# Kernel optimization log

Measured on AMD Instinct MI355X. Metric: run time of the kernel, lower is better.

The kernel has to match this reference:

```python
import jax, jax.numpy as jnp
import numpy as np

D_MODEL = 1024
NUM_HEADS = 16
HEAD_DIM = D_MODEL // NUM_HEADS


def setup_inputs() -> dict:
    key = jax.random.key(0)
    ks = jax.random.split(key, 11)
    B, S = 2, 2048
    s = 1.0 / np.sqrt(D_MODEL)
    return {
        "q": jax.random.normal(ks[0], (B, S, D_MODEL), jnp.float32),
        "k": jax.random.normal(ks[1], (B, S, D_MODEL), jnp.float32),
        "v": jax.random.normal(ks[2], (B, S, D_MODEL), jnp.float32),
        "Wq": jax.random.normal(ks[3], (D_MODEL, D_MODEL), jnp.float32) * s,
        "bq": jnp.zeros((D_MODEL,), jnp.float32),
        "Wk": jax.random.normal(ks[4], (D_MODEL, D_MODEL), jnp.float32) * s,
        "bk": jnp.zeros((D_MODEL,), jnp.float32),
        "Wv": jax.random.normal(ks[5], (D_MODEL, D_MODEL), jnp.float32) * s,
        "bv": jnp.zeros((D_MODEL,), jnp.float32),
        "Wo": jax.random.normal(ks[6], (D_MODEL, D_MODEL), jnp.float32) * s,
        "bo": jnp.zeros((D_MODEL,), jnp.float32),
    }


def _split_heads(x):
    B, S, _ = x.shape
    return x.reshape(B, S, NUM_HEADS, HEAD_DIM).transpose(0, 2, 1, 3)  # [B,H,S,Dh]


def reference(q, k, v, Wq, bq, Wk, bk, Wv, bv, Wo, bo):
    B, S, _ = q.shape
    qh = _split_heads(q @ Wq.T + bq)
    kh = _split_heads(k @ Wk.T + bk)
    vh = _split_heads(v @ Wv.T + bv)
    scale = 1.0 / jnp.sqrt(jnp.asarray(HEAD_DIM, qh.dtype))
    scores = jnp.einsum("bhqd,bhkd->bhqk", qh, kh) * scale  # [B,H,S,S]
    attn = jax.nn.softmax(scores, axis=-1)
    out = jnp.einsum("bhqk,bhkd->bhqd", attn, vh)
    out = out.transpose(0, 2, 1, 3).reshape(B, S, D_MODEL)
    return out @ Wo.T + bo
```

## Files before the change

kernel.cpp:

```cpp
#include <hip/hip_runtime.h>
#include <cstdint>
#include <cstddef>

#define DEVI __device__ __forceinline__

typedef short bf16x8 __attribute__((ext_vector_type(8)));
typedef short bf16x4 __attribute__((ext_vector_type(4)));
typedef float f32x4 __attribute__((ext_vector_type(4)));
typedef float f32x16 __attribute__((ext_vector_type(16)));
typedef unsigned short u16x4 __attribute__((ext_vector_type(4)));

constexpr int D_MODEL = 1024;
constexpr int HEADS = 16;
constexpr int DH = 64;
constexpr int SEQ = 2048;
constexpr int KDIM = 1024;

DEVI unsigned short f2bf(float f) {
  union { float f; unsigned u; } v; v.f = f;
  unsigned r = v.u + 0x7fffu + ((v.u >> 16) & 1u);
  return (unsigned short)(r >> 16);
}

DEVI unsigned pkbf(float a, float b) {
  return __builtin_amdgcn_perm(__float_as_uint(b), __float_as_uint(a), 0x07060302u);
}

DEVI void cp16(const void* g, void* l) {
  __builtin_amdgcn_global_load_lds(
      (const __attribute__((address_space(1))) void*)g,
      (__attribute__((address_space(3))) void*)l, 16, 0, 0);
}

DEVI f32x16 mfma_32x32x8(bf16x4 a, bf16x4 b, f32x16 c) {
#if __has_builtin(__builtin_amdgcn_mfma_f32_32x32x8bf16_1k)
  return __builtin_amdgcn_mfma_f32_32x32x8bf16_1k(a, b, c, 0, 0, 0);
#else
  asm volatile("v_mfma_f32_32x32x8_bf16 %0, %1, %2, %0" : "+v"(c) : "v"(a), "v"(b));
  return c;
#endif
}

__global__ void __launch_bounds__(256) castall(
    const float* __restrict__ q, const float* __restrict__ k, const float* __restrict__ v,
    const float* __restrict__ Wq, const float* __restrict__ Wk,
    const float* __restrict__ Wv, const float* __restrict__ Wo,
    unsigned short* __restrict__ qb, unsigned short* __restrict__ kb, unsigned short* __restrict__ vb,
    unsigned short* __restrict__ Wqb, unsigned short* __restrict__ Wkb,
    unsigned short* __restrict__ Wvb, unsigned short* __restrict__ Wob) {
  int bid = blockIdx.x;
  const float* s; unsigned short* d; int off;
  if (bid < 12288) {
    int w = bid >> 12; off = bid & 4095;
    s = (w == 0) ? q : ((w == 1) ? k : v);
    d = (w == 0) ? qb : ((w == 1) ? kb : vb);
  } else {
    int w = (bid - 12288) >> 10; off = bid & 1023;
    s = (w == 0) ? Wq : ((w == 1) ? Wk : ((w == 2) ? Wv : Wo));
    d = (w == 0) ? Wqb : ((w == 1) ? Wkb : ((w == 2) ? Wvb : Wob));
  }
  int i = (off * 256 + threadIdx.x) * 4;
  float4 x = *(const float4*)(s + i);
  u16x4 o; o[0] = f2bf(x.x); o[1] = f2bf(x.y); o[2] = f2bf(x.z); o[3] = f2bf(x.w);
  *(u16x4*)(d + i) = o;
}

DEVI void gemm_body64(const unsigned short* __restrict__ A, const unsigned short* __restrict__ W,
                      const float* __restrict__ bias, unsigned short* __restrict__ obf,
                      float* __restrict__ of32, float oscale, int mode, int bm, int bn,
                      unsigned short* As, unsigned short* Bs) {
  const int tid = threadIdx.x, lane = tid & 63, wave = tid >> 6;
  const int l16 = lane & 15, quad = lane >> 4;
  const int wn = wave * 32;
  const int sw = (l16 >> 1) & 3;
  f32x4 acc[4][2] = {};

  for (int k0 = 0; k0 < KDIM; k0 += 32) {
    {
      int row = tid >> 2, pblk = tid & 3;
      int col = (pblk ^ ((row >> 1) & 3)) * 8;
      cp16(A + (size_t)(bm * 64 + row) * KDIM + k0 + col, &As[tid * 8]);
    }
#pragma unroll
    for (int c = 0; c < 2; ++c) {
      int slot = c * 256 + tid;
      int row = slot >> 2, pblk = slot & 3;
      int col = (pblk ^ ((row >> 1) & 3)) * 8;
      cp16(W + (size_t)(bn * 128 + row) * KDIM + k0 + col, &Bs[slot * 8]);
    }
    asm volatile("s_waitcnt vmcnt(0)" ::: "memory");
    __syncthreads();
    bf16x8 af[4], bfr[2];
#pragma unroll
    for (int t = 0; t < 4; ++t)
      af[t] = *(const bf16x8*)&As[(t * 16 + l16) * 32 + ((quad ^ sw) * 8)];
#pragma unroll
    for (int u = 0; u < 2; ++u)
      bfr[u] = *(const bf16x8*)&Bs[(wn + u * 16 + l16) * 32 + ((quad ^ sw) * 8)];
#pragma unroll
    for (int i = 0; i < 4; ++i)
#pragma unroll
      for (int j = 0; j < 2; ++j)
        acc[i][j] = __builtin_amdgcn_mfma_f32_16x16x32_bf16(af[i], bfr[j], acc[i][j], 0, 0, 0);
    __syncthreads();
  }

#pragma unroll
  for (int i = 0; i < 4; ++i) {
#pragma unroll
    for (int j = 0; j < 2; ++j) {
      const int col = bn * 128 + wn + j * 16 + l16;
      const float bv = bias[col];
#pragma unroll
      for (int r = 0; r < 4; ++r) {
        const int row = bm * 64 + i * 16 + quad * 4 + r;
        const float val = (acc[i][j][r] + bv) * oscale;
        if (mode == 2) {
          of32[(size_t)row * D_MODEL + col] = val;
        } else {
          const int b = row >> 11, s = row & (SEQ - 1);
          const int h = col >> 6, d = col & (DH - 1);
          size_t idx;
          if (mode == 0) idx = ((size_t)(b * HEADS + h) * SEQ + s) * DH + d;
          else           idx = ((size_t)(b * HEADS + h) * DH + d) * SEQ + s;
          obf[idx] = f2bf(val);
        }
      }
    }
  }
}

__global__ void __launch_bounds__(256) qkv_gemm(
    const unsigned short* __restrict__ qb, const unsigned short* __restrict__ kb,
    const unsigned short* __restrict__ vb,
    const unsigned short* __restrict__ Wqb, const unsigned short* __restrict__ Wkb,
    const unsigned short* __restrict__ Wvb,
    const float* __restrict__ bq, const float* __restrict__ bk, const float* __restrict__ bv,
    unsigned short* __restrict__ Qh, unsigned short* __restrict__ Kh,
    unsigned short* __restrict__ Vt, float qscale) {
  __shared__ unsigned short As[64 * 32], Bs[128 * 32];
  const int bid = blockIdx.x, seg = bid >> 9, inner = bid & 511;
  const int bm = inner >> 3, bn = inner & 7;
  const unsigned short* A = (seg == 0) ? qb : ((seg == 1) ? kb : vb);
  const unsigned short* W = (seg == 0) ? Wqb : ((seg == 1) ? Wkb : Wvb);
  const float* bias = (seg == 0) ? bq : ((seg == 1) ? bk : bv);
  unsigned short* O = (seg == 0) ? Qh : ((seg == 1) ? Kh : Vt);
  gemm_body64(A, W, bias, O, nullptr, (seg == 0) ? qscale : 1.0f, (seg == 2) ? 1 : 0, bm, bn, As, Bs);
}

__global__ void __launch_bounds__(256) out_gemm(const unsigned short* __restrict__ AO,
                                                const unsigned short* __restrict__ Wob,
                                                const float* __restrict__ bo,
                                                float* __restrict__ out) {
  __shared__ unsigned short As[64 * 32], Bs[128 * 32];
  const int bid = blockIdx.x, bm = bid >> 3, bn = bid & 7;
  gemm_body64(AO, Wob, bo, nullptr, out, 1.0f, 2, bm, bn, As, Bs);
}

__global__ void __launch_bounds__(256) attn(const unsigned short* __restrict__ Qh,
                                            const unsigned short* __restrict__ Kh,
                                            const unsigned short* __restrict__ Vt,
                                            unsigned short* __restrict__ AO) {
  __shared__ __align__(16) char smem[32768];
  unsigned short* Ks = (unsigned short*)smem;
  unsigned short* Vs = (unsigned short*)(smem + 16384);

  const int bid = blockIdx.x;
  const int qt = bid >> 5, head = bid & 31, b = head >> 4, h = head & 15;
  const int tid = threadIdx.x;
  const int lane = tid & 63, wave = tid >> 6;
  const int wq = wave >> 1, wk = wave & 1;
  const int l31 = lane & 31, hh = lane >> 5;

  const unsigned short* Qhead = Qh + (size_t)(b * HEADS + h) * SEQ * DH;
  const unsigned short* Khead = Kh + (size_t)(b * HEADS + h) * SEQ * DH;
  const unsigned short* Vhead = Vt + (size_t)(b * HEADS + h) * DH * SEQ;

  const int qrow = qt * 64 + wq * 32 + l31;
  bf16x8 aq[4];
#pragma unroll
  for (int it = 0; it < 4; ++it)
    aq[it] = *(const bf16x8*)&Qhead[(size_t)qrow * DH + it * 16 + hh * 8];

  f32x16 oacc[2] = {};
  float lsum = 0.f;

  for (int kc = 0; kc < SEQ / 128; ++kc) {
#pragma unroll
    for (int c = 0; c < 4; ++c) {
      int s = c * 256 + tid;
      int row = s >> 3, pblk = s & 7;
      int jb = pblk ^ (row & 7);
      cp16(Khead + (size_t)(kc * 128 + row) * DH + jb * 8, &Ks[s * 8]);
    }
#pragma unroll
    for (int c = 0; c < 4; ++c) {
      int s = c * 256 + tid;
      int d = s >> 4, pblk = s & 15;
      int jb = pblk ^ (d & 7);
      cp16(Vhead + (size_t)d * SEQ + kc * 128 + jb * 8, &Vs[s * 8]);
    }
    asm volatile("s_waitcnt vmcnt(0)" ::: "memory");
    __syncthreads();

#pragma unroll
    for (int sub = 0; sub < 2; ++sub) {
      const int kb32 = sub * 64 + wk * 32;
      const int key = kb32 + l31;

      f32x16 sa = {};
#pragma unroll
      for (int it = 0; it < 4; ++it) {
        const int sblk = (2 * it + hh) ^ (key & 7);
        bf16x8 ak = *(const bf16x8*)&Ks[key * 64 + sblk * 8];
        sa = __builtin_amdgcn_mfma_f32_32x32x16_bf16(ak, aq[it], sa, 0, 0, 0);
      }

      float p[16];
#pragma unroll
      for (int r = 0; r < 16; ++r) {
        p[r] = __builtin_amdgcn_exp2f(sa[r]);
        lsum += p[r];
      }
      bf16x4 pk[4];
#pragma unroll
      for (int g = 0; g < 4; ++g) {
        union { unsigned u[2]; bf16x4 s; } c;
        c.u[0] = pkbf(p[4 * g + 0], p[4 * g + 1]);
        c.u[1] = pkbf(p[4 * g + 2], p[4 * g + 3]);
        pk[g] = c.s;
      }

#pragma unroll
      for (int g = 0; g < 4; ++g) {
        const int gblk = sub * 8 + wk * 4 + g;
#pragma unroll
        for (int dh2 = 0; dh2 < 2; ++dh2) {
          const int d = dh2 * 32 + l31;
          const int sv = gblk ^ (d & 7);
          bf16x4 av = *(const bf16x4*)&Vs[d * 128 + sv * 8 + hh * 4];
          oacc[dh2] = mfma_32x32x8(av, pk[g], oacc[dh2]);
        }
      }
    }
    __syncthreads();
  }

  lsum += __shfl_xor(lsum, 32);

  float* epiF = (float*)smem;
  float* lbuf = (float*)(smem + 16384);
  unsigned short* Oq = (unsigned short*)(smem + 17408);

  if (l31 == lane) lbuf[wave * 32 + l31] = lsum;
  if (wk == 1) {
#pragma unroll
    for (int dh2 = 0; dh2 < 2; ++dh2)
#pragma unroll
      for (int r = 0; r < 16; ++r) {
        const int d = dh2 * 32 + (r & 3) + 8 * (r >> 2) + 4 * hh;
        epiF[wq * 2048 + d * 32 + l31] = oacc[dh2][r];
      }
  }
  __syncthreads();

  if (wk == 0) {
    const float linv = 1.0f / (lsum + lbuf[(wq * 2 + 1) * 32 + l31]);
#pragma unroll
    for (int dh2 = 0; dh2 < 2; ++dh2) {
#pragma unroll
      for (int r = 0; r < 16; r += 2) {
        const int d = dh2 * 32 + (r & 3) + 8 * (r >> 2) + 4 * hh;
        const float v0 = (oacc[dh2][r]     + epiF[wq * 2048 + d * 32 + l31]) * linv;
        const float v1 = (oacc[dh2][r + 1] + epiF[wq * 2048 + (d + 1) * 32 + l31]) * linv;
        *(unsigned*)&Oq[wq * 2176 + l31 * 68 + d] = pkbf(v0, v1);
      }
    }
  }
  __syncthreads();

  {
    const int qloc = tid >> 2, d0 = (tid & 3) * 16;
    const int base = (qloc >> 5) * 2176 + (qloc & 31) * 68 + d0;
    unsigned u[8];
#pragma unroll
    for (int i = 0; i < 8; ++i) u[i] = *(const unsigned*)&Oq[base + i * 2];
    unsigned short* dst = AO + ((size_t)(b * SEQ + qt * 64 + qloc)) * D_MODEL + h * 64 + d0;
    *(uint4*)dst       = make_uint4(u[0], u[1], u[2], u[3]);
    *(uint4*)(dst + 8) = make_uint4(u[4], u[5], u[6], u[7]);
  }
}

extern "C" void kernel_launch(void* const* d_in, const int* in_sizes, int n_in,
                              void* d_out, int out_size, void* d_ws, size_t ws_size,
                              hipStream_t stream) {
  const float* q  = (const float*)d_in[0];
  const float* k  = (const float*)d_in[1];
  const float* v  = (const float*)d_in[2];
  const float* Wq = (const float*)d_in[3];
  const float* bq = (const float*)d_in[4];
  const float* Wk = (const float*)d_in[5];
  const float* bk = (const float*)d_in[6];
  const float* Wv = (const float*)d_in[7];
  const float* bv = (const float*)d_in[8];
  const float* Wo = (const float*)d_in[9];
  const float* bo = (const float*)d_in[10];
  float* out = (float*)d_out;

  char* ws = (char*)d_ws;
  const size_t MB = 1ull << 20;
  unsigned short* qb  = (unsigned short*)(ws + 0 * MB);
  unsigned short* kb  = (unsigned short*)(ws + 8 * MB);
  unsigned short* vb  = (unsigned short*)(ws + 16 * MB);
  unsigned short* Wqb = (unsigned short*)(ws + 24 * MB);
  unsigned short* Wkb = (unsigned short*)(ws + 26 * MB);
  unsigned short* Wvb = (unsigned short*)(ws + 28 * MB);
  unsigned short* Wob = (unsigned short*)(ws + 30 * MB);
  unsigned short* Qh  = (unsigned short*)(ws + 32 * MB);
  unsigned short* Kh  = (unsigned short*)(ws + 40 * MB);
  unsigned short* Vt  = (unsigned short*)(ws + 48 * MB);
  unsigned short* AO  = (unsigned short*)(ws + 56 * MB);

  castall<<<16384, 256, 0, stream>>>(q, k, v, Wq, Wk, Wv, Wo,
                                     qb, kb, vb, Wqb, Wkb, Wvb, Wob);

  const float qscale = 0.125f * 1.44269504088896f;
  qkv_gemm<<<1536, 256, 0, stream>>>(qb, kb, vb, Wqb, Wkb, Wvb, bq, bk, bv,
                                     Qh, Kh, Vt, qscale);

  attn<<<1024, 256, 0, stream>>>(Qh, Kh, Vt, AO);

  out_gemm<<<512, 256, 0, stream>>>(AO, Wob, bo, out);
}
```

Measured before the change: 253.2 us.

## Fuse fp32-to-bf16 activation cast into QKV GEMM with larger tiles

Removes the separate cast pass over q/k/v activations. The QKV GEMM now loads fp32 activations straight into shared memory using a swizzled layout and converts them to bf16 in registers before the MFMA. The GEMM tile also grows from 64x128 to 128x128 with a 2x2 wave layout, which halves the grid and improves reuse. In exchange it reads twice the activation bytes per tile, uses more LDS and registers, and adds per-iteration conversion ALU work. The out-projection GEMM is inlined unchanged.

```diff
diff --git a/kernel.cpp b/kernel.cpp
--- a/kernel.cpp
+++ b/kernel.cpp
@@ -24,6 +24,12 @@
 
 DEVI unsigned pkbf(float a, float b) {
   return __builtin_amdgcn_perm(__float_as_uint(b), __float_as_uint(a), 0x07060302u);
+}
+
+DEVI unsigned pkbf_rn(float a, float b) {
+  unsigned ua = __float_as_uint(a); ua += 0x7fffu + ((ua >> 16) & 1u);
+  unsigned ub = __float_as_uint(b); ub += 0x7fffu + ((ub >> 16) & 1u);
+  return __builtin_amdgcn_perm(ub, ua, 0x07060302u);
 }
 
 DEVI void cp16(const void* g, void* l) {
@@ -41,111 +47,107 @@
 #endif
 }
 
-__global__ void __launch_bounds__(256) castall(
-    const float* __restrict__ q, const float* __restrict__ k, const float* __restrict__ v,
+__global__ void __launch_bounds__(256) castW(
     const float* __restrict__ Wq, const float* __restrict__ Wk,
     const float* __restrict__ Wv, const float* __restrict__ Wo,
-    unsigned short* __restrict__ qb, unsigned short* __restrict__ kb, unsigned short* __restrict__ vb,
     unsigned short* __restrict__ Wqb, unsigned short* __restrict__ Wkb,
     unsigned short* __restrict__ Wvb, unsigned short* __restrict__ Wob) {
   int bid = blockIdx.x;
-  const float* s; unsigned short* d; int off;
-  if (bid < 12288) {
-    int w = bid >> 12; off = bid & 4095;
-    s = (w == 0) ? q : ((w == 1) ? k : v);
-    d = (w == 0) ? qb : ((w == 1) ? kb : vb);
-  } else {
-    int w = (bid - 12288) >> 10; off = bid & 1023;
-    s = (w == 0) ? Wq : ((w == 1) ? Wk : ((w == 2) ? Wv : Wo));
-    d = (w == 0) ? Wqb : ((w == 1) ? Wkb : ((w == 2) ? Wvb : Wob));
-  }
+  int w = bid >> 10, off = bid & 1023;
+  const float* s = (w == 0) ? Wq : ((w == 1) ? Wk : ((w == 2) ? Wv : Wo));
+  unsigned short* d = (w == 0) ? Wqb : ((w == 1) ? Wkb : ((w == 2) ? Wvb : Wob));
   int i = (off * 256 + threadIdx.x) * 4;
   float4 x = *(const float4*)(s + i);
   u16x4 o; o[0] = f2bf(x.x); o[1] = f2bf(x.y); o[2] = f2bf(x.z); o[3] = f2bf(x.w);
   *(u16x4*)(d + i) = o;
 }
 
-DEVI void gemm_body64(const unsigned short* __restrict__ A, const unsigned short* __restrict__ W,
-                      const float* __restrict__ bias, unsigned short* __restrict__ obf,
-                      float* __restrict__ of32, float oscale, int mode, int bm, int bn,
-                      unsigned short* As, unsigned short* Bs) {
-  const int tid = threadIdx.x, lane = tid & 63, wave = tid >> 6;
-  const int l16 = lane & 15, quad = lane >> 4;
-  const int wn = wave * 32;
-  const int sw = (l16 >> 1) & 3;
-  f32x4 acc[4][2] = {};
-
-  for (int k0 = 0; k0 < KDIM; k0 += 32) {
-    {
-      int row = tid >> 2, pblk = tid & 3;
-      int col = (pblk ^ ((row >> 1) & 3)) * 8;
-      cp16(A + (size_t)(bm * 64 + row) * KDIM + k0 + col, &As[tid * 8]);
-    }
-#pragma unroll
-    for (int c = 0; c < 2; ++c) {
-      int slot = c * 256 + tid;
-      int row = slot >> 2, pblk = slot & 3;
-      int col = (pblk ^ ((row >> 1) & 3)) * 8;
-      cp16(W + (size_t)(bn * 128 + row) * KDIM + k0 + col, &Bs[slot * 8]);
-    }
-    asm volatile("s_waitcnt vmcnt(0)" ::: "memory");
-    __syncthreads();
-    bf16x8 af[4], bfr[2];
-#pragma unroll
-    for (int t = 0; t < 4; ++t)
-      af[t] = *(const bf16x8*)&As[(t * 16 + l16) * 32 + ((quad ^ sw) * 8)];
-#pragma unroll
-    for (int u = 0; u < 2; ++u)
-      bfr[u] = *(const bf16x8*)&Bs[(wn + u * 16 + l16) * 32 + ((quad ^ sw) * 8)];
-#pragma unroll
-    for (int i = 0; i < 4; ++i)
-#pragma unroll
-      for (int j = 0; j < 2; ++j)
-        acc[i][j] = __builtin_amdgcn_mfma_f32_16x16x32_bf16(af[i], bfr[j], acc[i][j], 0, 0, 0);
-    __syncthreads();
-  }
-
-#pragma unroll
-  for (int i = 0; i < 4; ++i) {
-#pragma unroll
-    for (int j = 0; j < 2; ++j) {
-      const int col = bn * 128 + wn + j * 16 + l16;
-      const float bv = bias[col];
-#pragma unroll
-      for (int r = 0; r < 4; ++r) {
-        const int row = bm * 64 + i * 16 + quad * 4 + r;
-        const float val = (acc[i][j][r] + bv) * oscale;
-        if (mode == 2) {
-          of32[(size_t)row * D_MODEL + col] = val;
-        } else {
-          const int b = row >> 11, s = row & (SEQ - 1);
-          const int h = col >> 6, d = col & (DH - 1);
-          size_t idx;
-          if (mode == 0) idx = ((size_t)(b * HEADS + h) * SEQ + s) * DH + d;
-          else           idx = ((size_t)(b * HEADS + h) * DH + d) * SEQ + s;
-          obf[idx] = f2bf(val);
-        }
-      }
-    }
-  }
-}
-
 __global__ void __launch_bounds__(256) qkv_gemm(
-    const unsigned short* __restrict__ qb, const unsigned short* __restrict__ kb,
-    const unsigned short* __restrict__ vb,
+    const float* __restrict__ qf, const float* __restrict__ kf, const float* __restrict__ vf,
     const unsigned short* __restrict__ Wqb, const unsigned short* __restrict__ Wkb,
     const unsigned short* __restrict__ Wvb,
     const float* __restrict__ bq, const float* __restrict__ bk, const float* __restrict__ bv,
     unsigned short* __restrict__ Qh, unsigned short* __restrict__ Kh,
     unsigned short* __restrict__ Vt, float qscale) {
-  __shared__ unsigned short As[64 * 32], Bs[128 * 32];
-  const int bid = blockIdx.x, seg = bid >> 9, inner = bid & 511;
+  __shared__ float Asf[128 * 32];
+  __shared__ unsigned short Bs[128 * 32];
+  const int bid = blockIdx.x, seg = bid >> 8, inner = bid & 255;
   const int bm = inner >> 3, bn = inner & 7;
-  const unsigned short* A = (seg == 0) ? qb : ((seg == 1) ? kb : vb);
+  const float* A = (seg == 0) ? qf : ((seg == 1) ? kf : vf);
   const unsigned short* W = (seg == 0) ? Wqb : ((seg == 1) ? Wkb : Wvb);
   const float* bias = (seg == 0) ? bq : ((seg == 1) ? bk : bv);
   unsigned short* O = (seg == 0) ? Qh : ((seg == 1) ? Kh : Vt);
-  gemm_body64(A, W, bias, O, nullptr, (seg == 0) ? qscale : 1.0f, (seg == 2) ? 1 : 0, bm, bn, As, Bs);
+  const float oscale = (seg == 0) ? qscale : 1.0f;
+  const int mode = (seg == 2) ? 1 : 0;
+
+  const int tid = threadIdx.x, lane = tid & 63, wave = tid >> 6;
+  const int l16 = lane & 15, quad = lane >> 4;
+  const int wm = (wave >> 1) * 64, wn = (wave & 1) * 64;
+  const int sw = (l16 >> 1) & 3;
+  f32x4 acc[4][4] = {};
+
+  for (int k0 = 0; k0 < KDIM; k0 += 32) {
+#pragma unroll
+    for (int c = 0; c < 4; ++c) {
+      int slot = c * 256 + tid;
+      int row = slot >> 3, pb = slot & 7;
+      int jb = pb ^ (row & 7);
+      cp16(A + (size_t)(bm * 128 + row) * KDIM + k0 + jb * 4, &Asf[slot * 4]);
+    }
+#pragma unroll
+    for (int c = 0; c < 2; ++c) {
+      int slot = c * 256 + tid;
+      int row = slot >> 2, pb = slot & 3;
+      int col = (pb ^ ((row >> 1) & 3)) * 8;
+      cp16(W + (size_t)(bn * 128 + row) * KDIM + k0 + col, &Bs[slot * 8]);
+    }
+    asm volatile("s_waitcnt vmcnt(0)" ::: "memory");
+    __syncthreads();
+
+    bf16x8 af[4], bfr[4];
+#pragma unroll
+    for (int t = 0; t < 4; ++t) {
+      const int row = wm + t * 16 + l16;
+      const int s8 = row & 7;
+      f32x4 lo = *(const f32x4*)&Asf[row * 32 + ((2 * quad) ^ s8) * 4];
+      f32x4 hi = *(const f32x4*)&Asf[row * 32 + ((2 * quad + 1) ^ s8) * 4];
+      union { unsigned u[4]; bf16x8 v; } cvt;
+      cvt.u[0] = pkbf_rn(lo[0], lo[1]);
+      cvt.u[1] = pkbf_rn(lo[2], lo[3]);
+      cvt.u[2] = pkbf_rn(hi[0], hi[1]);
+      cvt.u[3] = pkbf_rn(hi[2], hi[3]);
+      af[t] = cvt.v;
+    }
+#pragma unroll
+    for (int t = 0; t < 4; ++t)
+      bfr[t] = *(const bf16x8*)&Bs[(wn + t * 16 + l16) * 32 + ((quad ^ sw) * 8)];
+#pragma unroll
+    for (int i = 0; i < 4; ++i)
+#pragma unroll
+      for (int j = 0; j < 4; ++j)
+        acc[i][j] = __builtin_amdgcn_mfma_f32_16x16x32_bf16(af[i], bfr[j], acc[i][j], 0, 0, 0);
+    __syncthreads();
+  }
+
+#pragma unroll
+  for (int i = 0; i < 4; ++i) {
+#pragma unroll
+    for (int j = 0; j < 4; ++j) {
+      const int col = bn * 128 + wn + j * 16 + l16;
+      const float bv = bias[col];
+#pragma unroll
+      for (int r = 0; r < 4; ++r) {
+        const int row = bm * 128 + wm + i * 16 + quad * 4 + r;
+        const float val = (acc[i][j][r] + bv) * oscale;
+        const int b = row >> 11, s = row & (SEQ - 1);
+        const int h = col >> 6, d = col & (DH - 1);
+        size_t idx;
+        if (mode == 0) idx = ((size_t)(b * HEADS + h) * SEQ + s) * DH + d;
+        else           idx = ((size_t)(b * HEADS + h) * DH + d) * SEQ + s;
+        O[idx] = f2bf(val);
+      }
+    }
+  }
 }
 
 __global__ void __launch_bounds__(256) out_gemm(const unsigned short* __restrict__ AO,
@@ -154,7 +156,54 @@
                                                 float* __restrict__ out) {
   __shared__ unsigned short As[64 * 32], Bs[128 * 32];
   const int bid = blockIdx.x, bm = bid >> 3, bn = bid & 7;
-  gemm_body64(AO, Wob, bo, nullptr, out, 1.0f, 2, bm, bn, As, Bs);
+  const int tid = threadIdx.x, lane = tid & 63, wave = tid >> 6;
+  const int l16 = lane & 15, quad = lane >> 4;
+  const int wn = wave * 32;
+  const int sw = (l16 >> 1) & 3;
+  f32x4 acc[4][2] = {};
+
+  for (int k0 = 0; k0 < KDIM; k0 += 32) {
+    {
+      int row = tid >> 2, pblk = tid & 3;
+      int col = (pblk ^ ((row >> 1) & 3)) * 8;
+      cp16(AO + (size_t)(bm * 64 + row) * KDIM + k0 + col, &As[tid * 8]);
+    }
+#pragma unroll
+    for (int c = 0; c < 2; ++c) {
+      int slot = c * 256 + tid;
+      int row = slot >> 2, pblk = slot & 3;
+      int col = (pblk ^ ((row >> 1) & 3)) * 8;
+      cp16(Wob + (size_t)(bn * 128 + row) * KDIM + k0 + col, &Bs[slot * 8]);
+    }
+    asm volatile("s_waitcnt vmcnt(0)" ::: "memory");
+    __syncthreads();
+    bf16x8 af[4], bfr[2];
+#pragma unroll
+    for (int t = 0; t < 4; ++t)
+      af[t] = *(const bf16x8*)&As[(t * 16 + l16) * 32 + ((quad ^ sw) * 8)];
+#pragma unroll
+    for (int u = 0; u < 2; ++u)
+      bfr[u] = *(const bf16x8*)&Bs[(wn + u * 16 + l16) * 32 + ((quad ^ sw) * 8)];
+#pragma unroll
+    for (int i = 0; i < 4; ++i)
+#pragma unroll
+      for (int j = 0; j < 2; ++j)
+        acc[i][j] = __builtin_amdgcn_mfma_f32_16x16x32_bf16(af[i], bfr[j], acc[i][j], 0, 0, 0);
+    __syncthreads();
+  }
+
+#pragma unroll
+  for (int i = 0; i < 4; ++i)
+#pragma unroll
+    for (int j = 0; j < 2; ++j) {
+      const int col = bn * 128 + wn + j * 16 + l16;
+      const float bv = bo[col];
+#pragma unroll
+      for (int r = 0; r < 4; ++r) {
+        const int row = bm * 64 + i * 16 + quad * 4 + r;
+        out[(size_t)row * D_MODEL + col] = acc[i][j][r] + bv;
+      }
+    }
 }
 
 __global__ void __launch_bounds__(256) attn(const unsigned short* __restrict__ Qh,
@@ -309,9 +358,6 @@
 
   char* ws = (char*)d_ws;
   const size_t MB = 1ull << 20;
-  unsigned short* qb  = (unsigned short*)(ws + 0 * MB);
-  unsigned short* kb  = (unsigned short*)(ws + 8 * MB);
-  unsigned short* vb  = (unsigned short*)(ws + 16 * MB);
   unsigned short* Wqb = (unsigned short*)(ws + 24 * MB);
   unsigned short* Wkb = (unsigned short*)(ws + 26 * MB);
   unsigned short* Wvb = (unsigned short*)(ws + 28 * MB);
@@ -321,12 +367,11 @@
   unsigned short* Vt  = (unsigned short*)(ws + 48 * MB);
   unsigned short* AO  = (unsigned short*)(ws + 56 * MB);
 
-  castall<<<16384, 256, 0, stream>>>(q, k, v, Wq, Wk, Wv, Wo,
-                                     qb, kb, vb, Wqb, Wkb, Wvb, Wob);
+  castW<<<4096, 256, 0, stream>>>(Wq, Wk, Wv, Wo, Wqb, Wkb, Wvb, Wob);
 
   const float qscale = 0.125f * 1.44269504088896f;
-  qkv_gemm<<<1536, 256, 0, stream>>>(qb, kb, vb, Wqb, Wkb, Wvb, bq, bk, bv,
-                                     Qh, Kh, Vt, qscale);
+  qkv_gemm<<<768, 256, 0, stream>>>(q, k, v, Wqb, Wkb, Wvb, bq, bk, bv,
+                                    Qh, Kh, Vt, qscale);
 
   attn<<<1024, 256, 0, stream>>>(Qh, Kh, Vt, AO);
 
```

Result: slower. 280.0 us (+10.6%).

## Double-buffer LDS in projection GEMMs and enlarge QKV tile to 128x128

Applied to the files above, without the earlier changes.

Both projection GEMMs now keep two LDS buffers and issue the next K-slice's global-to-LDS copies before computing on the current one, waiting only on the older loads. This hides global load latency behind MFMA work. The QKV GEMM also grows its block tile from 64x128 to 128x128 with a 2x2 wave layout, which improves operand reuse and halves the grid. The costs are more LDS and more accumulator registers per block, fewer blocks for the QKV launch, and a dependence on vmcnt ordering being correct.

```diff
diff --git a/kernel.cpp b/kernel.cpp
--- a/kernel.cpp
+++ b/kernel.cpp
@@ -40,6 +40,9 @@
   return c;
 #endif
 }
+
+#define BAR()        asm volatile("s_barrier" ::: "memory")
+#define WAITVM(n)    asm volatile("s_waitcnt vmcnt(" #n ")" ::: "memory")
 
 __global__ void __launch_bounds__(256) castall(
     const float* __restrict__ q, const float* __restrict__ k, const float* __restrict__ v,
@@ -65,71 +68,6 @@
   *(u16x4*)(d + i) = o;
 }
 
-DEVI void gemm_body64(const unsigned short* __restrict__ A, const unsigned short* __restrict__ W,
-                      const float* __restrict__ bias, unsigned short* __restrict__ obf,
-                      float* __restrict__ of32, float oscale, int mode, int bm, int bn,
-                      unsigned short* As, unsigned short* Bs) {
-  const int tid = threadIdx.x, lane = tid & 63, wave = tid >> 6;
-  const int l16 = lane & 15, quad = lane >> 4;
-  const int wn = wave * 32;
-  const int sw = (l16 >> 1) & 3;
-  f32x4 acc[4][2] = {};
-
-  for (int k0 = 0; k0 < KDIM; k0 += 32) {
-    {
-      int row = tid >> 2, pblk = tid & 3;
-      int col = (pblk ^ ((row >> 1) & 3)) * 8;
-      cp16(A + (size_t)(bm * 64 + row) * KDIM + k0 + col, &As[tid * 8]);
-    }
-#pragma unroll
-    for (int c = 0; c < 2; ++c) {
-      int slot = c * 256 + tid;
-      int row = slot >> 2, pblk = slot & 3;
-      int col = (pblk ^ ((row >> 1) & 3)) * 8;
-      cp16(W + (size_t)(bn * 128 + row) * KDIM + k0 + col, &Bs[slot * 8]);
-    }
-    asm volatile("s_waitcnt vmcnt(0)" ::: "memory");
-    __syncthreads();
-    bf16x8 af[4], bfr[2];
-#pragma unroll
-    for (int t = 0; t < 4; ++t)
-      af[t] = *(const bf16x8*)&As[(t * 16 + l16) * 32 + ((quad ^ sw) * 8)];
-#pragma unroll
-    for (int u = 0; u < 2; ++u)
-      bfr[u] = *(const bf16x8*)&Bs[(wn + u * 16 + l16) * 32 + ((quad ^ sw) * 8)];
-#pragma unroll
-    for (int i = 0; i < 4; ++i)
-#pragma unroll
-      for (int j = 0; j < 2; ++j)
-        acc[i][j] = __builtin_amdgcn_mfma_f32_16x16x32_bf16(af[i], bfr[j], acc[i][j], 0, 0, 0);
-    __syncthreads();
-  }
-
-#pragma unroll
-  for (int i = 0; i < 4; ++i) {
-#pragma unroll
-    for (int j = 0; j < 2; ++j) {
-      const int col = bn * 128 + wn + j * 16 + l16;
-      const float bv = bias[col];
-#pragma unroll
-      for (int r = 0; r < 4; ++r) {
-        const int row = bm * 64 + i * 16 + quad * 4 + r;
-        const float val = (acc[i][j][r] + bv) * oscale;
-        if (mode == 2) {
-          of32[(size_t)row * D_MODEL + col] = val;
-        } else {
-          const int b = row >> 11, s = row & (SEQ - 1);
-          const int h = col >> 6, d = col & (DH - 1);
-          size_t idx;
-          if (mode == 0) idx = ((size_t)(b * HEADS + h) * SEQ + s) * DH + d;
-          else           idx = ((size_t)(b * HEADS + h) * DH + d) * SEQ + s;
-          obf[idx] = f2bf(val);
-        }
-      }
-    }
-  }
-}
-
 __global__ void __launch_bounds__(256) qkv_gemm(
     const unsigned short* __restrict__ qb, const unsigned short* __restrict__ kb,
     const unsigned short* __restrict__ vb,
@@ -138,23 +76,155 @@
     const float* __restrict__ bq, const float* __restrict__ bk, const float* __restrict__ bv,
     unsigned short* __restrict__ Qh, unsigned short* __restrict__ Kh,
     unsigned short* __restrict__ Vt, float qscale) {
-  __shared__ unsigned short As[64 * 32], Bs[128 * 32];
-  const int bid = blockIdx.x, seg = bid >> 9, inner = bid & 511;
+  __shared__ unsigned short As[2][128 * 32];
+  __shared__ unsigned short Bs[2][128 * 32];
+  const int bid = blockIdx.x, seg = bid >> 8, inner = bid & 255;
   const int bm = inner >> 3, bn = inner & 7;
   const unsigned short* A = (seg == 0) ? qb : ((seg == 1) ? kb : vb);
   const unsigned short* W = (seg == 0) ? Wqb : ((seg == 1) ? Wkb : Wvb);
   const float* bias = (seg == 0) ? bq : ((seg == 1) ? bk : bv);
   unsigned short* O = (seg == 0) ? Qh : ((seg == 1) ? Kh : Vt);
-  gemm_body64(A, W, bias, O, nullptr, (seg == 0) ? qscale : 1.0f, (seg == 2) ? 1 : 0, bm, bn, As, Bs);
+  const float oscale = (seg == 0) ? qscale : 1.0f;
+  const int mode = (seg == 2) ? 1 : 0;
+
+  const int tid = threadIdx.x, lane = tid & 63, wave = tid >> 6;
+  const int l16 = lane & 15, quad = lane >> 4;
+  const int wm = (wave >> 1) * 64, wn = (wave & 1) * 64;
+  const int sw = (l16 >> 1) & 3;
+  f32x4 acc[4][4] = {};
+
+  const int r0 = tid >> 2, p0 = tid & 3;
+  const int c0 = (p0 ^ ((r0 >> 1) & 3)) * 8;
+  const int r1 = (256 + tid) >> 2, p1 = tid & 3;
+  const int c1 = (p1 ^ ((r1 >> 1) & 3)) * 8;
+  const unsigned short* Arow0 = A + (size_t)(bm * 128 + r0) * KDIM + c0;
+  const unsigned short* Arow1 = A + (size_t)(bm * 128 + r1) * KDIM + c1;
+  const unsigned short* Wrow0 = W + (size_t)(bn * 128 + r0) * KDIM + c0;
+  const unsigned short* Wrow1 = W + (size_t)(bn * 128 + r1) * KDIM + c1;
+
+#define QKV_ISSUE(K0, P)                                    \
+  do {                                                      \
+    cp16(Arow0 + (K0), &As[P][tid * 8]);                    \
+    cp16(Arow1 + (K0), &As[P][(256 + tid) * 8]);            \
+    cp16(Wrow0 + (K0), &Bs[P][tid * 8]);                    \
+    cp16(Wrow1 + (K0), &Bs[P][(256 + tid) * 8]);            \
+  } while (0)
+
+#define QKV_COMPUTE(P)                                                             \
+  do {                                                                             \
+    bf16x8 af[4], bfr[4];                                                          \
+    _Pragma("unroll") for (int t = 0; t < 4; ++t)                                  \
+        af[t] = *(const bf16x8*)&As[P][(wm + t * 16 + l16) * 32 + ((quad ^ sw) * 8)]; \
+    _Pragma("unroll") for (int t = 0; t < 4; ++t)                                  \
+        bfr[t] = *(const bf16x8*)&Bs[P][(wn + t * 16 + l16) * 32 + ((quad ^ sw) * 8)]; \
+    _Pragma("unroll") for (int i = 0; i < 4; ++i)                                  \
+        _Pragma("unroll") for (int j = 0; j < 4; ++j)                              \
+            acc[i][j] = __builtin_amdgcn_mfma_f32_16x16x32_bf16(af[i], bfr[j],     \
+                                                                acc[i][j], 0, 0, 0); \
+  } while (0)
+
+  QKV_ISSUE(0, 0);
+  for (int k = 0; k < 31; ++k) {
+    BAR();
+    QKV_ISSUE((k + 1) * 32, (k + 1) & 1);
+    WAITVM(4);
+    BAR();
+    if (k & 1) QKV_COMPUTE(1); else QKV_COMPUTE(0);
+  }
+  WAITVM(0);
+  BAR();
+  QKV_COMPUTE(1);
+
+#pragma unroll
+  for (int i = 0; i < 4; ++i) {
+#pragma unroll
+    for (int j = 0; j < 4; ++j) {
+      const int col = bn * 128 + wn + j * 16 + l16;
+      const float bv = bias[col];
+#pragma unroll
+      for (int r = 0; r < 4; ++r) {
+        const int row = bm * 128 + wm + i * 16 + quad * 4 + r;
+        const float val = (acc[i][j][r] + bv) * oscale;
+        const int b = row >> 11, s = row & (SEQ - 1);
+        const int h = col >> 6, d = col & (DH - 1);
+        size_t idx;
+        if (mode == 0) idx = ((size_t)(b * HEADS + h) * SEQ + s) * DH + d;
+        else           idx = ((size_t)(b * HEADS + h) * DH + d) * SEQ + s;
+        O[idx] = f2bf(val);
+      }
+    }
+  }
+#undef QKV_ISSUE
+#undef QKV_COMPUTE
 }
 
 __global__ void __launch_bounds__(256) out_gemm(const unsigned short* __restrict__ AO,
                                                 const unsigned short* __restrict__ Wob,
                                                 const float* __restrict__ bo,
                                                 float* __restrict__ out) {
-  __shared__ unsigned short As[64 * 32], Bs[128 * 32];
+  __shared__ unsigned short As[2][64 * 32];
+  __shared__ unsigned short Bs[2][128 * 32];
   const int bid = blockIdx.x, bm = bid >> 3, bn = bid & 7;
-  gemm_body64(AO, Wob, bo, nullptr, out, 1.0f, 2, bm, bn, As, Bs);
+  const int tid = threadIdx.x, lane = tid & 63, wave = tid >> 6;
+  const int l16 = lane & 15, quad = lane >> 4;
+  const int wn = wave * 32;
+  const int sw = (l16 >> 1) & 3;
+  f32x4 acc[4][2] = {};
+
+  const int ra = tid >> 2, pa = tid & 3;
+  const int ca = (pa ^ ((ra >> 1) & 3)) * 8;
+  const int r1 = (256 + tid) >> 2;
+  const int c1 = (pa ^ ((r1 >> 1) & 3)) * 8;
+  const unsigned short* Arow  = AO + (size_t)(bm * 64 + ra) * KDIM + ca;
+  const unsigned short* Wrow0 = Wob + (size_t)(bn * 128 + ra) * KDIM + ca;
+  const unsigned short* Wrow1 = Wob + (size_t)(bn * 128 + r1) * KDIM + c1;
+
+#define OUT_ISSUE(K0, P)                                    \
+  do {                                                      \
+    cp16(Arow + (K0), &As[P][tid * 8]);                     \
+    cp16(Wrow0 + (K0), &Bs[P][tid * 8]);                    \
+    cp16(Wrow1 + (K0), &Bs[P][(256 + tid) * 8]);            \
+  } while (0)
+
+#define OUT_COMPUTE(P)                                                             \
+  do {                                                                             \
+    bf16x8 af[4], bfr[2];                                                          \
+    _Pragma("unroll") for (int t = 0; t < 4; ++t)                                  \
+        af[t] = *(const bf16x8*)&As[P][(t * 16 + l16) * 32 + ((quad ^ sw) * 8)];   \
+    _Pragma("unroll") for (int u = 0; u < 2; ++u)                                  \
+        bfr[u] = *(const bf16x8*)&Bs[P][(wn + u * 16 + l16) * 32 + ((quad ^ sw) * 8)]; \
+    _Pragma("unroll") for (int i = 0; i < 4; ++i)                                  \
+        _Pragma("unroll") for (int j = 0; j < 2; ++j)                              \
+            acc[i][j] = __builtin_amdgcn_mfma_f32_16x16x32_bf16(af[i], bfr[j],     \
+                                                                acc[i][j], 0, 0, 0); \
+  } while (0)
+
+  OUT_ISSUE(0, 0);
+  for (int k = 0; k < 31; ++k) {
+    BAR();
+    OUT_ISSUE((k + 1) * 32, (k + 1) & 1);
+    WAITVM(3);
+    BAR();
+    if (k & 1) OUT_COMPUTE(1); else OUT_COMPUTE(0);
+  }
+  WAITVM(0);
+  BAR();
+  OUT_COMPUTE(1);
+
+#pragma unroll
+  for (int i = 0; i < 4; ++i)
+#pragma unroll
+    for (int j = 0; j < 2; ++j) {
+      const int col = bn * 128 + wn + j * 16 + l16;
+      const float bv = bo[col];
+#pragma unroll
+      for (int r = 0; r < 4; ++r) {
+        const int row = bm * 64 + i * 16 + quad * 4 + r;
+        out[(size_t)row * D_MODEL + col] = acc[i][j][r] + bv;
+      }
+    }
+#undef OUT_ISSUE
+#undef OUT_COMPUTE
 }
 
 __global__ void __launch_bounds__(256) attn(const unsigned short* __restrict__ Qh,
@@ -325,8 +395,8 @@
                                      qb, kb, vb, Wqb, Wkb, Wvb, Wob);
 
   const float qscale = 0.125f * 1.44269504088896f;
-  qkv_gemm<<<1536, 256, 0, stream>>>(qb, kb, vb, Wqb, Wkb, Wvb, bq, bk, bv,
-                                     Qh, Kh, Vt, qscale);
+  qkv_gemm<<<768, 256, 0, stream>>>(qb, kb, vb, Wqb, Wkb, Wvb, bq, bk, bv,
+                                    Qh, Kh, Vt, qscale);
 
   attn<<<1024, 256, 0, stream>>>(Qh, Kh, Vt, AO);
 
```

After: 257.2 us. No clear change (+1.6%).
